# Kernel optimization log

Hardware: AMD Instinct MI355X
Metric: run time of the kernel (lower is better)

## Reference

```python
import jax, jax.numpy as jnp
import numpy as np

BATCH, IN_DIM, HID_DIM, OUT_DIM, K = 8192, 256, 16384, 256, 256


def setup_inputs() -> dict:
    key = jax.random.key(0)
    k1, k2, k3 = jax.random.split(key, 3)
    x = jax.random.normal(k1, (BATCH, IN_DIM), dtype=jnp.float32)
    # kaiming_uniform-like init scale for encoder/decoder weights
    enc_w = jax.random.normal(k2, (HID_DIM, IN_DIM), dtype=jnp.float32) * (1.0 / np.sqrt(IN_DIM))
    enc_b = jnp.zeros((HID_DIM,), dtype=jnp.float32)
    dec_w = jax.random.normal(k3, (OUT_DIM, HID_DIM), dtype=jnp.float32) * (1.0 / np.sqrt(HID_DIM))
    dec_b = jnp.zeros((OUT_DIM,), dtype=jnp.float32)
    return {"x": x, "enc_w": enc_w, "enc_b": enc_b, "dec_w": dec_w, "dec_b": dec_b, "k": K}


def reference(x, enc_w, enc_b, dec_w, dec_b, k):
    # encoder: [B, in] @ [in, hid] -> [B, hid]
    hidden_pre = x @ enc_w.T + enc_b
    h_relu = jax.nn.relu(hidden_pre)
    kk = min(h_relu.shape[1], int(k))
    # k-th largest value per row as threshold; mask = (x_relu >= threshold)
    topk_vals, _ = jax.lax.top_k(h_relu, kk)          # [B, k]
    thresholds = topk_vals[:, -1:]                    # [B, 1]
    hidden_post = jnp.where(h_relu >= thresholds, h_relu, 0.0)
    # decoder: [B, hid] @ [hid, out] -> [B, out]
    output = hidden_post @ dec_w.T + dec_b
    return (output, hidden_post)
```

## Files before the change

kernel.cpp:

```cpp
#include <hip/hip_runtime.h>
#include <stdint.h>

#define BATCH   8192
#define IN_DIM  256
#define HID_DIM 16384
#define OUT_DIM 256

#define SELCAPF 2048
#define TKBINS  4096
#define TKCAND  512

typedef __attribute__((ext_vector_type(4))) float f32x4;
typedef __attribute__((ext_vector_type(2))) float f32x2;

__device__ __forceinline__ float bf16u_to_f(unsigned short u) {
  return __uint_as_float(((unsigned)u) << 16);
}
__device__ __forceinline__ unsigned short f_to_bf16_rne(float f) {
  unsigned u = __float_as_uint(f);
  u += 0x7fffu + ((u >> 16) & 1u);
  return (unsigned short)(u >> 16);
}
__device__ __forceinline__ int read_k(const int* kptr) {
  int k = kptr[0];
  if (k <= 0 || k > 100000000) {
    float kf = __int_as_float(k);
    if (kf >= 1.f && kf <= 16384.f) k = (int)kf;
  }
  if (k < 1) k = 1;
  if (k > HID_DIM) k = HID_DIM;
  return k;
}
__device__ __forceinline__ f32x2 fma2(f32x2 a, f32x2 b, f32x2 c) {
#if __has_builtin(__builtin_elementwise_fma)
  return __builtin_elementwise_fma(a, b, c);
#else
  f32x2 r; r[0] = fmaf(a[0], b[0], c[0]); r[1] = fmaf(a[1], b[1], c[1]); return r;
#endif
}

__global__ __launch_bounds__(256) void k_transb(const float* __restrict__ dec_w,
                                                unsigned short* __restrict__ decT) {
  __shared__ float tile[32][33];
  int j0 = blockIdx.x * 32, o0 = blockIdx.y * 32;
  int tx = threadIdx.x & 31, ty = threadIdx.x >> 5;
#pragma unroll
  for (int rr = 0; rr < 4; rr++)
    tile[ty + rr * 8][tx] = dec_w[(size_t)(o0 + ty + rr * 8) * HID_DIM + (j0 + tx)];
  __syncthreads();
#pragma unroll
  for (int rr = 0; rr < 4; rr++)
    decT[(size_t)(j0 + ty + rr * 8) * OUT_DIM + (o0 + tx)] = f_to_bf16_rne(tile[tx][ty + rr * 8]);
}

__global__ __launch_bounds__(256, 4) void k_gemm_pk(const float* __restrict__ X,
                                                    const float* __restrict__ W,
                                                    const float* __restrict__ encb,
                                                    float* __restrict__ hid) {
  __shared__ float As[32][132];
  __shared__ float Bs[32][132];
  const int bn = blockIdx.x, bm = blockIdx.y;
  const int t = threadIdx.x;
  const int tx = t & 15, ty = t >> 4;
  const int sr = t & 127, sh = t >> 7;

  f32x2 acc[8][4] = {};

  const float* Ab = X + (size_t)(bm * 128) * IN_DIM;
  const float* Bb = W + (size_t)(bn * 128) * IN_DIM;

  for (int k0 = 0; k0 < IN_DIM; k0 += 32) {
#pragma unroll
    for (int q = 0; q < 4; q++) {
      const int ko = sh * 16 + q * 4;
      const float4 av = *(const float4*)&Ab[(size_t)sr * IN_DIM + k0 + ko];
      As[ko + 0][sr] = av.x; As[ko + 1][sr] = av.y;
      As[ko + 2][sr] = av.z; As[ko + 3][sr] = av.w;
      const float4 bv = *(const float4*)&Bb[(size_t)sr * IN_DIM + k0 + ko];
      Bs[ko + 0][sr] = bv.x; Bs[ko + 1][sr] = bv.y;
      Bs[ko + 2][sr] = bv.z; Bs[ko + 3][sr] = bv.w;
    }
    __syncthreads();
#pragma unroll 8
    for (int kk = 0; kk < 32; kk++) {
      float a[8]; f32x2 b2[4];
      *(float4*)&a[0] = *(const float4*)&As[kk][ty * 8];
      *(float4*)&a[4] = *(const float4*)&As[kk][ty * 8 + 4];
      const float4 b0 = *(const float4*)&Bs[kk][tx * 8];
      const float4 b1 = *(const float4*)&Bs[kk][tx * 8 + 4];
      b2[0][0] = b0.x; b2[0][1] = b0.y; b2[1][0] = b0.z; b2[1][1] = b0.w;
      b2[2][0] = b1.x; b2[2][1] = b1.y; b2[3][0] = b1.z; b2[3][1] = b1.w;
#pragma unroll
      for (int i = 0; i < 8; i++) {
        f32x2 ai; ai[0] = a[i]; ai[1] = a[i];
#pragma unroll
        for (int j = 0; j < 4; j++)
          acc[i][j] = fma2(ai, b2[j], acc[i][j]);
      }
    }
    __syncthreads();
  }

#pragma unroll
  for (int i = 0; i < 8; i++) {
    const int m = bm * 128 + ty * 8 + i;
    float o[8];
#pragma unroll
    for (int j = 0; j < 4; j++) {
      const float h0 = acc[i][j][0] + encb[bn * 128 + tx * 8 + j * 2];
      const float h1 = acc[i][j][1] + encb[bn * 128 + tx * 8 + j * 2 + 1];
      o[j * 2]     = (h0 > 0.f) ? h0 : 0.f;
      o[j * 2 + 1] = (h1 > 0.f) ? h1 : 0.f;
    }
    float* dst = &hid[(size_t)m * HID_DIM + bn * 128 + tx * 8];
    *(float4*)dst = *(float4*)&o[0];
    *(float4*)(dst + 4) = *(float4*)&o[4];
  }
}

__global__ __launch_bounds__(256) void k_topk4(const unsigned short* __restrict__ decTb,
                                               const float* __restrict__ decb,
                                               const int* __restrict__ kptr,
                                               float* __restrict__ out,
                                               float* __restrict__ hid) {
  __shared__ unsigned hist[TKBINS];
  __shared__ unsigned part[257];
  __shared__ unsigned candB[TKCAND];
  __shared__ unsigned short candI[TKCAND];
  __shared__ float selV[SELCAPF];
  __shared__ unsigned short selI[SELCAPF];
  __shared__ unsigned s_selcnt, s_cnt, s_T, s_need, s_bin;
  __shared__ int s_keepall;

  const int r = blockIdx.x, t = threadIdx.x;
  float* hrow = hid + (size_t)r * HID_DIM;
  const int k = read_k(kptr);

  f32x4 row[16];
#pragma unroll
  for (int c = 0; c < 16; c++) row[c] = *(const f32x4*)&hrow[(c * 256 + t) * 4];

  for (int i = t; i < TKBINS; i += 256) hist[i] = 0u;
  if (t == 0) { s_selcnt = 0; s_cnt = 0; s_keepall = 0; s_T = 0; }
  __syncthreads();

#pragma unroll
  for (int c = 0; c < 16; c++)
#pragma unroll
    for (int e = 0; e < 4; e++) {
      const unsigned bin = __float_as_uint(row[c][e]) >> 19;
      if (bin) atomicAdd(&hist[bin], 1u);
    }
  __syncthreads();

  { unsigned s = 0; const int b0 = t * 16;
#pragma unroll
    for (int u = 0; u < 16; u++) s += hist[b0 + u];
    part[t] = s; }
  __syncthreads();
  for (int off = 1; off < 256; off <<= 1) {
    const unsigned v = part[t];
    const unsigned a = (t + off < 256) ? part[t + off] : 0u;
    __syncthreads();
    part[t] = v + a;
    __syncthreads();
  }
  if (t == 0 && part[0] < (unsigned)k) s_keepall = 1;
  {
    const unsigned incl = part[t], excl = (t < 255) ? part[t + 1] : 0u;
    if (incl >= (unsigned)k && excl < (unsigned)k) {
      unsigned cum = excl; int bin = t * 16; unsigned need = 1;
      for (int b = t * 16 + 15; b >= t * 16; b--) {
        const unsigned c2 = hist[b];
        if (cum + c2 >= (unsigned)k) { bin = b; need = (unsigned)k - cum; break; }
        cum += c2;
      }
      s_bin = (unsigned)bin; s_need = need;
    }
  }
  __syncthreads();

  const int keepall = s_keepall;
  unsigned T = 0u;
  if (!keepall) {
    int shift = 19;
    unsigned prefix = s_bin;
    for (;;) {
      if (t == 0) s_cnt = 0;
      __syncthreads();
#pragma unroll
      for (int c = 0; c < 16; c++)
#pragma unroll
        for (int e = 0; e < 4; e++) {
          const unsigned bits = __float_as_uint(row[c][e]);
          if ((bits >> shift) == prefix) {
            const unsigned p = atomicAdd(&s_cnt, 1u);
            if (p < TKCAND) { candB[p] = bits; candI[p] = (unsigned short)((c * 256 + t) * 4 + e); }
          }
        }
      __syncthreads();
      if (s_cnt <= TKCAND || shift == 0) break;
      const int nsh = (shift >= 4) ? shift - 4 : 0;
      const int nb = shift - nsh;
      if (t < (1 << nb)) part[t] = 0u;
      __syncthreads();
#pragma unroll
      for (int c = 0; c < 16; c++)
#pragma unroll
        for (int e = 0; e < 4; e++) {
          const unsigned bits = __float_as_uint(row[c][e]);
          if ((bits >> shift) == prefix)
            atomicAdd(&part[(bits >> nsh) & ((1u << nb) - 1u)], 1u);
        }
      __syncthreads();
      if (t == 0) {
        unsigned cum = 0; const unsigned need = s_need;
        for (int b = (1 << nb) - 1; b >= 0; b--) {
          const unsigned c2 = part[b];
          if (cum + c2 >= need) { s_bin = (unsigned)b; s_need = need - cum; break; }
          cum += c2;
        }
      }
      __syncthreads();
      prefix = (prefix << nb) | s_bin;
      shift = nsh;
      __syncthreads();
    }
    if (shift == 0) {
      if (t == 0) s_T = prefix;
    } else {
      const unsigned n = s_cnt;
      const unsigned need = s_need;
      for (unsigned i = t; i < n; i += 256) {
        const unsigned v = candB[i];
        unsigned g = 0, e = 0;
        for (unsigned j = 0; j < n; j++) {
          const unsigned u = candB[j];
          g += (u > v); e += (u == v);
        }
        if (g < need && need <= g + e) s_T = v;
      }
    }
    __syncthreads();
    T = s_T;
  }

#pragma unroll
  for (int c = 0; c < 16; c++) {
    const int base = (c * 256 + t) * 4;
    f32x4 o;
#pragma unroll
    for (int e = 0; e < 4; e++) {
      const float v = row[c][e];
      const unsigned bits = __float_as_uint(v);
      const bool keep = keepall || (bits >= T);
      o[e] = keep ? v : 0.f;
      if (keep && bits != 0u) {
        const unsigned p = atomicAdd(&s_selcnt, 1u);
        if (p < SELCAPF) { selV[p] = v; selI[p] = (unsigned short)(base + e); }
      }
    }
    *(f32x4*)&hrow[base] = o;
  }
  __syncthreads();

  const unsigned nsel = s_selcnt;
  float a0 = decb[t], a1 = 0.f, a2 = 0.f, a3 = 0.f;
  if (nsel <= SELCAPF) {
    unsigned s = 0;
    for (; s + 4 <= nsel; s += 4) {
      a0 += selV[s + 0] * bf16u_to_f(decTb[(size_t)selI[s + 0] * OUT_DIM + t]);
      a1 += selV[s + 1] * bf16u_to_f(decTb[(size_t)selI[s + 1] * OUT_DIM + t]);
      a2 += selV[s + 2] * bf16u_to_f(decTb[(size_t)selI[s + 2] * OUT_DIM + t]);
      a3 += selV[s + 3] * bf16u_to_f(decTb[(size_t)selI[s + 3] * OUT_DIM + t]);
    }
    for (; s < nsel; s++)
      a0 += selV[s] * bf16u_to_f(decTb[(size_t)selI[s] * OUT_DIM + t]);
  } else {
    for (int j = 0; j < HID_DIM; j++) {
      const float hv = hrow[j];
      if (hv != 0.f) a0 += hv * bf16u_to_f(decTb[(size_t)j * OUT_DIM + t]);
    }
  }
  out[(size_t)r * OUT_DIM + t] = (a0 + a1) + (a2 + a3);
}

__global__ __launch_bounds__(256) void k_topkf(const float* __restrict__ dec,
                                               const float* __restrict__ decb,
                                               const int* __restrict__ kptr,
                                               float* __restrict__ out,
                                               float* __restrict__ hid) {
  __shared__ unsigned hist[8][257];
  __shared__ unsigned tot[256];
  __shared__ float selV[SELCAPF];
  __shared__ unsigned short selI[SELCAPF];
  __shared__ unsigned s_selcnt, s_need, s_pref, s_byte;
  __shared__ int s_keepall;

  const int r = blockIdx.x, t = threadIdx.x;
  float* hrow = hid + (size_t)r * HID_DIM;
  const int k = read_k(kptr);

  for (int i = t; i < 8 * 257; i += 256) ((unsigned*)hist)[i] = 0u;
  if (t == 0) { s_selcnt = 0; s_keepall = 0; s_pref = 0; }
  __syncthreads();
#pragma unroll
  for (int c = 0; c < 16; c++) {
    const f32x4 v = *(const f32x4*)&hrow[(c * 256 + t) * 4];
#pragma unroll
    for (int e = 0; e < 4; e++) {
      const unsigned b = __float_as_uint(v[e]) >> 24;
      if (b) atomicAdd(&hist[t & 7][b], 1u);
    }
  }
  __syncthreads();
  { unsigned s = 0;
#pragma unroll
    for (int c = 0; c < 8; c++) s += hist[c][t];
    tot[t] = s; }
  __syncthreads();
  if (t == 0) {
    unsigned cum = 0; int b1 = -1; unsigned need = 0;
    for (int b = 255; b >= 1; b--) {
      const unsigned c = tot[b];
      if (cum + c >= (unsigned)k) { b1 = b; need = (unsigned)k - cum; break; }
      cum += c;
    }
    if (b1 < 0) s_keepall = 1;
    else { s_pref = ((unsigned)b1) << 24; s_need = need; }
  }
  __syncthreads();
  if (!s_keepall) {
    for (int pass = 1; pass <= 3; pass++) {
      const int shift = 24 - pass * 8;
      tot[t] = 0;
      __syncthreads();
      const unsigned prefhi = s_pref >> (shift + 8);
#pragma unroll
      for (int c = 0; c < 16; c++) {
        const f32x4 v = *(const f32x4*)&hrow[(c * 256 + t) * 4];
#pragma unroll
        for (int e = 0; e < 4; e++) {
          const unsigned bits = __float_as_uint(v[e]);
          if ((bits >> (shift + 8)) == prefhi) atomicAdd(&tot[(bits >> shift) & 255u], 1u);
        }
      }
      __syncthreads();
      if (t == 0) {
        unsigned cum = 0; const unsigned need = s_need;
        for (int b = 255; b >= 0; b--) {
          const unsigned c = tot[b];
          if (cum + c >= need) { s_byte = (unsigned)b; s_need = need - cum; break; }
          cum += c;
        }
        s_pref |= s_byte << shift;
      }
      __syncthreads();
    }
  }
  const int keepall = s_keepall;
  const unsigned T = s_pref;
#pragma unroll
  for (int c = 0; c < 16; c++) {
    const int base = (c * 256 + t) * 4;
    const f32x4 v = *(const f32x4*)&hrow[base];
    f32x4 o;
#pragma unroll
    for (int e = 0; e < 4; e++) {
      const unsigned bits = __float_as_uint(v[e]);
      const bool keep = keepall || (bits >= T);
      o[e] = keep ? v[e] : 0.f;
      if (keep && bits != 0u) {
        const unsigned p = atomicAdd(&s_selcnt, 1u);
        if (p < SELCAPF) { selV[p] = v[e]; selI[p] = (unsigned short)(base + e); }
      }
    }
    *(f32x4*)&hrow[base] = o;
  }
  __syncthreads();
  const unsigned nsel = s_selcnt;
  float a0 = decb[t], a1 = 0.f, a2 = 0.f, a3 = 0.f;
  if (nsel <= SELCAPF) {
    unsigned s = 0;
    for (; s + 4 <= nsel; s += 4) {
#pragma unroll
      for (int u = 0; u < 4; u++) {
        const unsigned idx = selI[s + u];
        (u == 0 ? a0 : u == 1 ? a1 : u == 2 ? a2 : a3) += selV[s + u] * dec[(size_t)t * HID_DIM + idx];
      }
    }
    for (; s < nsel; s++)
      a0 += selV[s] * dec[(size_t)t * HID_DIM + selI[s]];
  } else {
    for (int j = 0; j < HID_DIM; j++) {
      const float hv = hrow[j];
      if (hv != 0.f) a0 += hv * dec[(size_t)t * HID_DIM + j];
    }
  }
  out[(size_t)r * OUT_DIM + t] = (a0 + a1) + (a2 + a3);
}

extern "C" void kernel_launch(void* const* d_in, const int* in_sizes, int n_in,
                              void* d_out, int out_size, void* d_ws, size_t ws_size,
                              hipStream_t stream) {
  int ix = 0, iew = 1, ieb = 2, idw = 3, idb = 4, ik = 5;
  if (n_in >= 6 && in_sizes[0] == OUT_DIM && in_sizes[5] == BATCH * IN_DIM) {
    idb = 0; idw = 1; ieb = 2; iew = 3; ik = 4; ix = 5;
  }
  const float* x     = (const float*)d_in[ix];
  const float* enc_w = (const float*)d_in[iew];
  const float* enc_b = (const float*)d_in[ieb];
  const float* dec_w = (const float*)d_in[idw];
  const float* dec_b = (const float*)d_in[idb];
  const int*   kptr  = (const int*)d_in[ik];

  float* out = (float*)d_out;
  float* hid = out + (size_t)BATCH * OUT_DIM;

  k_gemm_pk<<<dim3(HID_DIM / 128, BATCH / 128), 256, 0, stream>>>(x, enc_w, enc_b, hid);

  const size_t B_decT = (size_t)HID_DIM * OUT_DIM * 2;
  if (ws_size >= 64 + B_decT) {
    unsigned short* decTb = (unsigned short*)((char*)d_ws + 64);
    k_transb<<<dim3(HID_DIM / 32, OUT_DIM / 32), 256, 0, stream>>>(dec_w, decTb);
    k_topk4<<<dim3(BATCH), 256, 0, stream>>>(decTb, dec_b, kptr, out, hid);
  } else {
    k_topkf<<<dim3(BATCH), 256, 0, stream>>>(dec_w, dec_b, kptr, out, hid);
  }
}
```

Measured before the change: 1.599 ms.

## Pre-transpose GEMM operands and stage tiles via direct global-to-LDS loads; simplify top-k radix

Adds transpose kernels that lay out x and enc_w in k-major 128-wide blocks in workspace, so the encoder GEMM can fill shared memory with global_load_lds 16-byte copies instead of register-staged transposing stores. The top-k kernel switches to an 8-bit first radix pass with replicated histograms and a larger candidate buffer that no longer stores indices. The sparse decoder loop is unrolled to 8 accumulators. The cost is two extra transpose launches and more workspace traffic, and the padded LDS layout is dropped, which may bring back bank conflicts.

```diff
diff --git a/kernel.cpp b/kernel.cpp
--- a/kernel.cpp
+++ b/kernel.cpp
@@ -7,12 +7,16 @@
 #define OUT_DIM 256
 
 #define SELCAPF 2048
-#define TKBINS  4096
-#define TKCAND  512
+#define TKCAP   2048
 
 typedef __attribute__((ext_vector_type(4))) float f32x4;
 typedef __attribute__((ext_vector_type(2))) float f32x2;
 
+__device__ __forceinline__ void load_lds_16B(const void* g, void* l) {
+  __builtin_amdgcn_global_load_lds(
+      (const __attribute__((address_space(1))) unsigned int*)g,
+      (__attribute__((address_space(3))) unsigned int*)l, 16, 0, 0);
+}
 __device__ __forceinline__ float bf16u_to_f(unsigned short u) {
   return __uint_as_float(((unsigned)u) << 16);
 }
@@ -53,46 +57,61 @@
     decT[(size_t)(j0 + ty + rr * 8) * OUT_DIM + (o0 + tx)] = f_to_bf16_rne(tile[tx][ty + rr * 8]);
 }
 
-__global__ __launch_bounds__(256, 4) void k_gemm_pk(const float* __restrict__ X,
-                                                    const float* __restrict__ W,
-                                                    const float* __restrict__ encb,
-                                                    float* __restrict__ hid) {
-  __shared__ float As[32][132];
-  __shared__ float Bs[32][132];
+__global__ __launch_bounds__(256) void k_transblk(const float* __restrict__ src,
+                                                  float* __restrict__ dst) {
+  __shared__ float tile[32][33];
+  const int r0 = blockIdx.x * 32, k0 = blockIdx.y * 32;
+  const int tx = threadIdx.x & 31, ty = threadIdx.x >> 5;
+#pragma unroll
+  for (int rr = 0; rr < 4; rr++)
+    tile[ty + rr * 8][tx] = src[(size_t)(r0 + ty + rr * 8) * IN_DIM + (k0 + tx)];
+  __syncthreads();
+  const int blk = r0 >> 7, rin = r0 & 127;
+#pragma unroll
+  for (int rr = 0; rr < 4; rr++) {
+    const int kk = k0 + ty + rr * 8;
+    dst[((size_t)blk * IN_DIM + kk) * 128 + rin + tx] = tile[tx][ty + rr * 8];
+  }
+}
+
+__global__ __launch_bounds__(256, 4) void k_gemm_pk2(const float* __restrict__ XT,
+                                                     const float* __restrict__ WT,
+                                                     const float* __restrict__ encb,
+                                                     float* __restrict__ hid) {
+  __shared__ __align__(16) float As[32 * 128];
+  __shared__ __align__(16) float Bs[32 * 128];
   const int bn = blockIdx.x, bm = blockIdx.y;
-  const int t = threadIdx.x;
+  const int t = threadIdx.x, w = t >> 6, lane = t & 63;
   const int tx = t & 15, ty = t >> 4;
-  const int sr = t & 127, sh = t >> 7;
 
   f32x2 acc[8][4] = {};
 
-  const float* Ab = X + (size_t)(bm * 128) * IN_DIM;
-  const float* Bb = W + (size_t)(bn * 128) * IN_DIM;
+  const float* Abase = XT + (size_t)bm * (IN_DIM * 128);
+  const float* Bbase = WT + (size_t)bn * (IN_DIM * 128);
 
   for (int k0 = 0; k0 < IN_DIM; k0 += 32) {
 #pragma unroll
-    for (int q = 0; q < 4; q++) {
-      const int ko = sh * 16 + q * 4;
-      const float4 av = *(const float4*)&Ab[(size_t)sr * IN_DIM + k0 + ko];
-      As[ko + 0][sr] = av.x; As[ko + 1][sr] = av.y;
-      As[ko + 2][sr] = av.z; As[ko + 3][sr] = av.w;
-      const float4 bv = *(const float4*)&Bb[(size_t)sr * IN_DIM + k0 + ko];
-      Bs[ko + 0][sr] = bv.x; Bs[ko + 1][sr] = bv.y;
-      Bs[ko + 2][sr] = bv.z; Bs[ko + 3][sr] = bv.w;
+    for (int o = 0; o < 4; o++) {
+      const int i = w * 4 + o;
+      load_lds_16B(Abase + k0 * 128 + i * 256 + lane * 4, &As[i * 256]);
+      load_lds_16B(Bbase + k0 * 128 + i * 256 + lane * 4, &Bs[i * 256]);
     }
     __syncthreads();
 #pragma unroll 8
     for (int kk = 0; kk < 32; kk++) {
-      float a[8]; f32x2 b2[4];
-      *(float4*)&a[0] = *(const float4*)&As[kk][ty * 8];
-      *(float4*)&a[4] = *(const float4*)&As[kk][ty * 8 + 4];
-      const float4 b0 = *(const float4*)&Bs[kk][tx * 8];
-      const float4 b1 = *(const float4*)&Bs[kk][tx * 8 + 4];
-      b2[0][0] = b0.x; b2[0][1] = b0.y; b2[1][0] = b0.z; b2[1][1] = b0.w;
-      b2[2][0] = b1.x; b2[2][1] = b1.y; b2[3][0] = b1.z; b2[3][1] = b1.w;
+      const f32x4 av0 = *(const f32x4*)&As[kk * 128 + ty * 8];
+      const f32x4 av1 = *(const f32x4*)&As[kk * 128 + ty * 8 + 4];
+      const f32x4 bv0 = *(const f32x4*)&Bs[kk * 128 + tx * 8];
+      const f32x4 bv1 = *(const f32x4*)&Bs[kk * 128 + tx * 8 + 4];
+      f32x2 b2[4];
+      b2[0] = __builtin_shufflevector(bv0, bv0, 0, 1);
+      b2[1] = __builtin_shufflevector(bv0, bv0, 2, 3);
+      b2[2] = __builtin_shufflevector(bv1, bv1, 0, 1);
+      b2[3] = __builtin_shufflevector(bv1, bv1, 2, 3);
 #pragma unroll
       for (int i = 0; i < 8; i++) {
-        f32x2 ai; ai[0] = a[i]; ai[1] = a[i];
+        const float asc = (i < 4) ? av0[i & 3] : av1[i & 3];
+        f32x2 ai; ai[0] = asc; ai[1] = asc;
 #pragma unroll
         for (int j = 0; j < 4; j++)
           acc[i][j] = fma2(ai, b2[j], acc[i][j]);
@@ -118,18 +137,17 @@
   }
 }
 
-__global__ __launch_bounds__(256) void k_topk4(const unsigned short* __restrict__ decTb,
+__global__ __launch_bounds__(256) void k_topk5(const unsigned short* __restrict__ decTb,
                                                const float* __restrict__ decb,
                                                const int* __restrict__ kptr,
                                                float* __restrict__ out,
                                                float* __restrict__ hid) {
-  __shared__ unsigned hist[TKBINS];
-  __shared__ unsigned part[257];
-  __shared__ unsigned candB[TKCAND];
-  __shared__ unsigned short candI[TKCAND];
+  __shared__ unsigned hist[8][257];
+  __shared__ unsigned cums[257];
+  __shared__ unsigned candB[TKCAP];
   __shared__ float selV[SELCAPF];
   __shared__ unsigned short selI[SELCAPF];
-  __shared__ unsigned s_selcnt, s_cnt, s_T, s_need, s_bin;
+  __shared__ unsigned s_selcnt, s_cnt, s_need, s_T, s_bin, s_B;
   __shared__ int s_keepall;
 
   const int r = blockIdx.x, t = threadIdx.x;
@@ -140,7 +158,7 @@
 #pragma unroll
   for (int c = 0; c < 16; c++) row[c] = *(const f32x4*)&hrow[(c * 256 + t) * 4];
 
-  for (int i = t; i < TKBINS; i += 256) hist[i] = 0u;
+  for (int i = t; i < 8 * 257; i += 256) ((unsigned*)hist)[i] = 0u;
   if (t == 0) { s_selcnt = 0; s_cnt = 0; s_keepall = 0; s_T = 0; }
   __syncthreads();
 
@@ -148,43 +166,34 @@
   for (int c = 0; c < 16; c++)
 #pragma unroll
     for (int e = 0; e < 4; e++) {
-      const unsigned bin = __float_as_uint(row[c][e]) >> 19;
-      if (bin) atomicAdd(&hist[bin], 1u);
-    }
-  __syncthreads();
-
-  { unsigned s = 0; const int b0 = t * 16;
-#pragma unroll
-    for (int u = 0; u < 16; u++) s += hist[b0 + u];
-    part[t] = s; }
+      const unsigned b = __float_as_uint(row[c][e]) >> 24;
+      if (b) atomicAdd(&hist[t & 7][b], 1u);
+    }
+  __syncthreads();
+  { unsigned s = 0;
+#pragma unroll
+    for (int cpy = 0; cpy < 8; cpy++) s += hist[cpy][t];
+    cums[t] = s; }
   __syncthreads();
   for (int off = 1; off < 256; off <<= 1) {
-    const unsigned v = part[t];
-    const unsigned a = (t + off < 256) ? part[t + off] : 0u;
-    __syncthreads();
-    part[t] = v + a;
-    __syncthreads();
-  }
-  if (t == 0 && part[0] < (unsigned)k) s_keepall = 1;
-  {
-    const unsigned incl = part[t], excl = (t < 255) ? part[t + 1] : 0u;
-    if (incl >= (unsigned)k && excl < (unsigned)k) {
-      unsigned cum = excl; int bin = t * 16; unsigned need = 1;
-      for (int b = t * 16 + 15; b >= t * 16; b--) {
-        const unsigned c2 = hist[b];
-        if (cum + c2 >= (unsigned)k) { bin = b; need = (unsigned)k - cum; break; }
-        cum += c2;
-      }
-      s_bin = (unsigned)bin; s_need = need;
-    }
+    const unsigned v = cums[t];
+    const unsigned a = (t + off < 256) ? cums[t + off] : 0u;
+    __syncthreads();
+    cums[t] = v + a;
+    __syncthreads();
+  }
+  if (t == 0 && cums[1] < (unsigned)k) s_keepall = 1;
+  if (t >= 1) {
+    const unsigned incl = cums[t], excl = (t < 255) ? cums[t + 1] : 0u;
+    if (incl >= (unsigned)k && excl < (unsigned)k) { s_B = (unsigned)t; s_need = (unsigned)k - excl; }
   }
   __syncthreads();
 
   const int keepall = s_keepall;
   unsigned T = 0u;
   if (!keepall) {
-    int shift = 19;
-    unsigned prefix = s_bin;
+    unsigned prefix = s_B;
+    int shift = 24;
     for (;;) {
       if (t == 0) s_cnt = 0;
       __syncthreads();
@@ -195,38 +204,36 @@
           const unsigned bits = __float_as_uint(row[c][e]);
           if ((bits >> shift) == prefix) {
             const unsigned p = atomicAdd(&s_cnt, 1u);
-            if (p < TKCAND) { candB[p] = bits; candI[p] = (unsigned short)((c * 256 + t) * 4 + e); }
+            if (p < TKCAP) candB[p] = bits;
           }
         }
       __syncthreads();
-      if (s_cnt <= TKCAND || shift == 0) break;
-      const int nsh = (shift >= 4) ? shift - 4 : 0;
-      const int nb = shift - nsh;
-      if (t < (1 << nb)) part[t] = 0u;
+      if (s_cnt <= TKCAP || shift == 0) break;
+      const int nsh = shift - 4;
+      if (t < 16) cums[t] = 0u;
       __syncthreads();
 #pragma unroll
       for (int c = 0; c < 16; c++)
 #pragma unroll
         for (int e = 0; e < 4; e++) {
           const unsigned bits = __float_as_uint(row[c][e]);
-          if ((bits >> shift) == prefix)
-            atomicAdd(&part[(bits >> nsh) & ((1u << nb) - 1u)], 1u);
+          if ((bits >> shift) == prefix) atomicAdd(&cums[(bits >> nsh) & 15u], 1u);
         }
       __syncthreads();
       if (t == 0) {
         unsigned cum = 0; const unsigned need = s_need;
-        for (int b = (1 << nb) - 1; b >= 0; b--) {
-          const unsigned c2 = part[b];
+        for (int b = 15; b >= 0; b--) {
+          const unsigned c2 = cums[b];
           if (cum + c2 >= need) { s_bin = (unsigned)b; s_need = need - cum; break; }
           cum += c2;
         }
       }
       __syncthreads();
-      prefix = (prefix << nb) | s_bin;
+      prefix = (prefix << 4) | s_bin;
       shift = nsh;
       __syncthreads();
     }
-    if (shift == 0) {
+    if (shift == 0 && s_cnt > TKCAP) {
       if (t == 0) s_T = prefix;
     } else {
       const unsigned n = s_cnt;
@@ -265,14 +272,18 @@
   __syncthreads();
 
   const unsigned nsel = s_selcnt;
-  float a0 = decb[t], a1 = 0.f, a2 = 0.f, a3 = 0.f;
+  float a0 = decb[t], a1 = 0.f, a2 = 0.f, a3 = 0.f, a4 = 0.f, a5 = 0.f, a6 = 0.f, a7 = 0.f;
   if (nsel <= SELCAPF) {
     unsigned s = 0;
-    for (; s + 4 <= nsel; s += 4) {
+    for (; s + 8 <= nsel; s += 8) {
       a0 += selV[s + 0] * bf16u_to_f(decTb[(size_t)selI[s + 0] * OUT_DIM + t]);
       a1 += selV[s + 1] * bf16u_to_f(decTb[(size_t)selI[s + 1] * OUT_DIM + t]);
       a2 += selV[s + 2] * bf16u_to_f(decTb[(size_t)selI[s + 2] * OUT_DIM + t]);
       a3 += selV[s + 3] * bf16u_to_f(decTb[(size_t)selI[s + 3] * OUT_DIM + t]);
+      a4 += selV[s + 4] * bf16u_to_f(decTb[(size_t)selI[s + 4] * OUT_DIM + t]);
+      a5 += selV[s + 5] * bf16u_to_f(decTb[(size_t)selI[s + 5] * OUT_DIM + t]);
+      a6 += selV[s + 6] * bf16u_to_f(decTb[(size_t)selI[s + 6] * OUT_DIM + t]);
+      a7 += selV[s + 7] * bf16u_to_f(decTb[(size_t)selI[s + 7] * OUT_DIM + t]);
     }
     for (; s < nsel; s++)
       a0 += selV[s] * bf16u_to_f(decTb[(size_t)selI[s] * OUT_DIM + t]);
@@ -282,7 +293,70 @@
       if (hv != 0.f) a0 += hv * bf16u_to_f(decTb[(size_t)j * OUT_DIM + t]);
     }
   }
-  out[(size_t)r * OUT_DIM + t] = (a0 + a1) + (a2 + a3);
+  out[(size_t)r * OUT_DIM + t] = (((a0 + a1) + (a2 + a3)) + ((a4 + a5) + (a6 + a7)));
+}
+
+__global__ __launch_bounds__(256, 4) void k_gemm_pk(const float* __restrict__ X,
+                                                    const float* __restrict__ W,
+                                                    const float* __restrict__ encb,
+                                                    float* __restrict__ hid) {
+  __shared__ float As[32][132];
+  __shared__ float Bs[32][132];
+  const int bn = blockIdx.x, bm = blockIdx.y;
+  const int t = threadIdx.x;
+  const int tx = t & 15, ty = t >> 4;
+  const int sr = t & 127, sh = t >> 7;
+  f32x2 acc[8][4] = {};
+  const float* Ab = X + (size_t)(bm * 128) * IN_DIM;
+  const float* Bb = W + (size_t)(bn * 128) * IN_DIM;
+  for (int k0 = 0; k0 < IN_DIM; k0 += 32) {
+#pragma unroll
+    for (int q = 0; q < 4; q++) {
+      const int ko = sh * 16 + q * 4;
+      const float4 av = *(const float4*)&Ab[(size_t)sr * IN_DIM + k0 + ko];
+      As[ko + 0][sr] = av.x; As[ko + 1][sr] = av.y;
+      As[ko + 2][sr] = av.z; As[ko + 3][sr] = av.w;
+      const float4 bv = *(const float4*)&Bb[(size_t)sr * IN_DIM + k0 + ko];
+      Bs[ko + 0][sr] = bv.x; Bs[ko + 1][sr] = bv.y;
+      Bs[ko + 2][sr] = bv.z; Bs[ko + 3][sr] = bv.w;
+    }
+    __syncthreads();
+#pragma unroll 8
+    for (int kk = 0; kk < 32; kk++) {
+      const f32x4 av0 = *(const f32x4*)&As[kk][ty * 8];
+      const f32x4 av1 = *(const f32x4*)&As[kk][ty * 8 + 4];
+      const f32x4 bv0 = *(const f32x4*)&Bs[kk][tx * 8];
+      const f32x4 bv1 = *(const f32x4*)&Bs[kk][tx * 8 + 4];
+      f32x2 b2[4];
+      b2[0] = __builtin_shufflevector(bv0, bv0, 0, 1);
+      b2[1] = __builtin_shufflevector(bv0, bv0, 2, 3);
+      b2[2] = __builtin_shufflevector(bv1, bv1, 0, 1);
+      b2[3] = __builtin_shufflevector(bv1, bv1, 2, 3);
+#pragma unroll
+      for (int i = 0; i < 8; i++) {
+        const float asc = (i < 4) ? av0[i & 3] : av1[i & 3];
+        f32x2 ai; ai[0] = asc; ai[1] = asc;
+#pragma unroll
+        for (int j = 0; j < 4; j++) acc[i][j] = fma2(ai, b2[j], acc[i][j]);
+      }
+    }
+    __syncthreads();
+  }
+#pragma unroll
+  for (int i = 0; i < 8; i++) {
+    const int m = bm * 128 + ty * 8 + i;
+    float o[8];
+#pragma unroll
+    for (int j = 0; j < 4; j++) {
+      const float h0 = acc[i][j][0] + encb[bn * 128 + tx * 8 + j * 2];
+      const float h1 = acc[i][j][1] + encb[bn * 128 + tx * 8 + j * 2 + 1];
+      o[j * 2] = (h0 > 0.f) ? h0 : 0.f;
+      o[j * 2 + 1] = (h1 > 0.f) ? h1 : 0.f;
+    }
+    float* dst = &hid[(size_t)m * HID_DIM + bn * 128 + tx * 8];
+    *(float4*)dst = *(float4*)&o[0];
+    *(float4*)(dst + 4) = *(float4*)&o[4];
+  }
 }
 
 __global__ __launch_bounds__(256) void k_topkf(const float* __restrict__ dec,
@@ -296,11 +370,9 @@
   __shared__ unsigned short selI[SELCAPF];
   __shared__ unsigned s_selcnt, s_need, s_pref, s_byte;
   __shared__ int s_keepall;
-
   const int r = blockIdx.x, t = threadIdx.x;
   float* hrow = hid + (size_t)r * HID_DIM;
   const int k = read_k(kptr);
-
   for (int i = t; i < 8 * 257; i += 256) ((unsigned*)hist)[i] = 0u;
   if (t == 0) { s_selcnt = 0; s_keepall = 0; s_pref = 0; }
   __syncthreads();
@@ -417,14 +489,23 @@
   float* out = (float*)d_out;
   float* hid = out + (size_t)BATCH * OUT_DIM;
 
-  k_gemm_pk<<<dim3(HID_DIM / 128, BATCH / 128), 256, 0, stream>>>(x, enc_w, enc_b, hid);
-
   const size_t B_decT = (size_t)HID_DIM * OUT_DIM * 2;
-  if (ws_size >= 64 + B_decT) {
-    unsigned short* decTb = (unsigned short*)((char*)d_ws + 64);
+  const size_t B_XT   = (size_t)BATCH * IN_DIM * 4;
+  const size_t B_WT   = (size_t)HID_DIM * IN_DIM * 4;
+  const size_t need = 64 + B_decT + B_XT + B_WT;
+
+  if (ws_size >= need) {
+    unsigned char* p = (unsigned char*)d_ws;
+    unsigned short* decTb = (unsigned short*)(p + 64);
+    float* XT = (float*)(p + 64 + B_decT);
+    float* WT = (float*)(p + 64 + B_decT + B_XT);
+    k_transblk<<<dim3(BATCH / 32, IN_DIM / 32), 256, 0, stream>>>(x, XT);
+    k_transblk<<<dim3(HID_DIM / 32, IN_DIM / 32), 256, 0, stream>>>(enc_w, WT);
     k_transb<<<dim3(HID_DIM / 32, OUT_DIM / 32), 256, 0, stream>>>(dec_w, decTb);
-    k_topk4<<<dim3(BATCH), 256, 0, stream>>>(decTb, dec_b, kptr, out, hid);
+    k_gemm_pk2<<<dim3(HID_DIM / 128, BATCH / 128), 256, 0, stream>>>(XT, WT, enc_b, hid);
+    k_topk5<<<dim3(BATCH), 256, 0, stream>>>(decTb, dec_b, kptr, out, hid);
   } else {
+    k_gemm_pk<<<dim3(HID_DIM / 128, BATCH / 128), 256, 0, stream>>>(x, enc_w, enc_b, hid);
     k_topkf<<<dim3(BATCH), 256, 0, stream>>>(dec_w, dec_b, kptr, out, hid);
   }
 }
```

Measured after the change: 1.717 ms. 1.07x slower.
